# Kernel tuning notes

Hardware: AMD Instinct MI355X
Metric: run time of the kernel (lower is better)

Reference implementation:

```python
import jax, jax.numpy as jnp
import numpy as np

N, C, H, W = 4, 64, 64, 64
K = 3


def _unfold(x, k):
    """torch F.unfold with padding k//2: [n,c,h,w] -> [n, c*k*k, h*w].
    Feature ordering matches torch: index = c*k*k + i*k + j."""
    p = k // 2
    n, c, h, w = x.shape
    xp = jnp.pad(x, ((0, 0), (0, 0), (p, p), (p, p)))
    patches = jnp.stack(
        [xp[:, :, i:i + h, j:j + w] for i in range(k) for j in range(k)], axis=2
    )  # [n, c, k*k, h, w]
    return patches.reshape(n, c * k * k, h * w)


def _mask_vec(c, k):
    # causal patch mask from __init__: zero out center-and-right of middle row and all rows below
    m = np.ones((c, k, k), np.float32)
    m[:, k // 2, k // 2:] = 0
    m[:, k // 2 + 1:, :] = 0
    return jnp.asarray(m.reshape(1, c * k * k, 1))


def setup_inputs() -> dict:
    key = jax.random.key(0)
    k1, k2 = jax.random.split(key)
    y_hat = jax.random.normal(k1, (N, C, H, W), dtype=jnp.float32)
    y_prob = jax.random.uniform(k2, (N, 1, H, W), dtype=jnp.float32)
    return {"y_hat": y_hat, "y_prob": y_prob}


def reference(y_hat, y_prob):
    k = K
    n, c, h, w = y_hat.shape
    L = h * w
    mask = _mask_vec(c, k)

    u = _unfold(y_hat, k) * mask                              # [n, c*k*k, L]
    u = u / jnp.maximum(jnp.linalg.norm(u, axis=1, keepdims=True), 1e-12)
    R = jnp.einsum('nfl,nfm->nlm', u, u)                      # [n, L, L] cosine sims

    # eval path: keep strictly-upper triangle (causal: l < m)
    row = jnp.arange(L)[:, None]
    col = jnp.arange(L)[None, :]
    R = jnp.where(col > row, R, 0.0)

    R_star = jnp.max(R, axis=1)                               # [n, L]
    arg = jnp.argmax(R, axis=1).astype(jnp.int32)             # [n, L]

    y_unf = _unfold(y_hat, k)                                 # [n, c*k*k, L]
    ref_unfold = jnp.take_along_axis(y_unf, arg[:, None, :], axis=2)

    prob_unf = y_prob.reshape(n, -1, L)                       # 1x1 unfold
    U_unf = jnp.take_along_axis(prob_unf, arg[:, None, :], axis=2)

    S = R_star.reshape(n, 1, h, w)
    U = U_unf.reshape(n, -1, h, w)

    # eval-mode position-0 overrides
    S = S.at[:, :, 0, 0].set(1e-8)
    U = U.at[:, :, 0, 0].set(1e-8)
    ref_unfold = ref_unfold.at[:, :, 0].set(0.0)
    arg = arg.at[:, 0].set(-1)

    S = jnp.clip(S, 1e-8, 1.0)
    U = jnp.clip(U, 1e-8, 1.0)
    return S, U, ref_unfold, arg
```

## Files before the change

### kernel.cpp

```cpp
#include <hip/hip_runtime.h>
#include <stdint.h>

#define Nn 4
#define Cc 64
#define LL 4096
#define KK 256
#define TRI2 528

typedef _Float16 half8 __attribute__((ext_vector_type(8)));
typedef float f32x16 __attribute__((ext_vector_type(16)));
typedef float f4a __attribute__((ext_vector_type(4), aligned(4)));
typedef unsigned short ushort8v __attribute__((ext_vector_type(8)));

__device__ __forceinline__ unsigned f2ord(float f) {
    unsigned u = __float_as_uint(f);
    return u ^ ((u & 0x80000000u) ? 0xFFFFFFFFu : 0x80000000u);
}
__device__ __forceinline__ float ord2f(unsigned o) {
    unsigned u = (o & 0x80000000u) ? (o ^ 0x80000000u) : ~o;
    return __uint_as_float(u);
}
__device__ __forceinline__ unsigned short h2u(_Float16 h) {
    union { _Float16 f; unsigned short u; } x; x.f = h; return x.u;
}

__global__ __launch_bounds__(256) void build_v(const float* __restrict__ yhat,
                                               unsigned short* __restrict__ VhT,
                                               unsigned short* __restrict__ VlT,
                                               unsigned long long* __restrict__ best) {
    int blk = blockIdx.x;
    int xcd = blk & 7;
    int n = xcd >> 1;
    int i64 = (blk >> 3) + (xcd & 1) * 128;
    int tid = threadIdx.x;
    if (tid < 16) best[(size_t)n * LL + i64 * 16 + tid] = 0ull;

    int cg = tid & 15;
    int l = i64 * 16 + (tid >> 4);
    int y = l >> 6, x = l & 63;
    const float* src = yhat + (size_t)n * (Cc * LL);

    float vals[16];
    float sumsq = 0.f;
#pragma unroll
    for (int ci = 0; ci < 4; ++ci) {
        const float* p = src + (cg * 4 + ci) * LL;
        float t0 = (y > 0 && x > 0)  ? p[l - 65] : 0.f;
        float t1 = (y > 0)           ? p[l - 64] : 0.f;
        float t2 = (y > 0 && x < 63) ? p[l - 63] : 0.f;
        float t3 = (x > 0)           ? p[l - 1]  : 0.f;
        vals[ci * 4 + 0] = t0; vals[ci * 4 + 1] = t1;
        vals[ci * 4 + 2] = t2; vals[ci * 4 + 3] = t3;
        sumsq += t0 * t0 + t1 * t1 + t2 * t2 + t3 * t3;
    }
    sumsq += __shfl_xor(sumsq, 1, 64);
    sumsq += __shfl_xor(sumsq, 2, 64);
    sumsq += __shfl_xor(sumsq, 4, 64);
    sumsq += __shfl_xor(sumsq, 8, 64);
    float inv = 1.f / fmaxf(sqrtf(sumsq), 1e-12f);

    size_t pk = ((((size_t)n * 128 + (l >> 5)) * 16 + cg) << 9) + (l & 31) * 8;
    unsigned short* dh = VhT + pk;
    unsigned short* dl = VlT + pk;
    ushort8v hA, hB, lA, lB;
#pragma unroll
    for (int kk = 0; kk < 16; ++kk) {
        float v = vals[kk] * inv;
        _Float16 h = (fabsf(v) < 6.1035e-5f) ? (_Float16)0 : (_Float16)v;
        _Float16 lo = (_Float16)((v - (float)h) * 2048.0f);
        unsigned short hu = h2u(h * (_Float16)2048.0f);
        unsigned short lu = h2u(lo);
        if (kk < 8) { hA[kk] = hu; lA[kk] = lu; }
        else        { hB[kk - 8] = hu; lB[kk - 8] = lu; }
    }
    *(ushort8v*)(dh)       = hA;
    *(ushort8v*)(dh + 256) = hB;
    *(ushort8v*)(dl)       = lA;
    *(ushort8v*)(dl + 256) = lB;
}

__global__ __launch_bounds__(256) void simmax(const unsigned short* __restrict__ Vh,
                                              const unsigned short* __restrict__ Vl,
                                              unsigned long long* __restrict__ best) {
    int bx = blockIdx.x;
    int xcd = bx & 7, idx = bx >> 3;
    int n = xcd >> 1;
    int t = (xcd & 1) * 264 + idx;
    int j = (int)((sqrtf(8.f * (float)t + 1.f) - 1.f) * 0.5f);
    while ((j + 1) * (j + 2) / 2 <= t) ++j;
    while (j * (j + 1) / 2 > t) --j;
    int i = t - j * (j + 1) / 2;
    int l0 = i * 128, m0 = j * 128;

    int tid = threadIdx.x;
    int w = tid >> 6, lane = tid & 63;
    int r5 = lane & 31, h5 = lane >> 5;
    int rw = (w & 1) * 64;
    int cw = (w >> 1) * 64;
    if ((i == j) && (rw == 64) && (cw == 0)) return;

    const unsigned short* VhB = Vh + (size_t)n * (LL * KK);
    const unsigned short* VlB = Vl + (size_t)n * (LL * KK);

    const unsigned short* A_hi = VhB + ((size_t)((l0 + rw) >> 5) << 13) + lane * 8;
    const unsigned short* A_lo = VlB + ((size_t)((l0 + rw) >> 5) << 13) + lane * 8;
    const unsigned short* B_hi = VhB + ((size_t)((m0 + cw) >> 5) << 13) + lane * 8;
    const unsigned short* B_lo = VlB + ((size_t)((m0 + cw) >> 5) << 13) + lane * 8;

    f32x16 acc[2][2];
#pragma unroll
    for (int r = 0; r < 2; ++r)
#pragma unroll
        for (int c = 0; c < 2; ++c) acc[r][c] = (f32x16)0.f;

#pragma unroll 1
    for (int kb = 0; kb < 16; kb += 2) {
        half8 fal[2][2], fah[2][2], fbl[2][2], fbh[2][2];
#pragma unroll
        for (int kc = 0; kc < 2; ++kc)
#pragma unroll
            for (int r = 0; r < 2; ++r) {
                fal[r][kc] = *(const half8*)(A_lo + ((r * 16 + kb + kc) << 9));
                fbh[r][kc] = *(const half8*)(B_hi + ((r * 16 + kb + kc) << 9));
            }
#pragma unroll
        for (int kc = 0; kc < 2; ++kc)
#pragma unroll
            for (int r = 0; r < 2; ++r) {
                fah[r][kc] = *(const half8*)(A_hi + ((r * 16 + kb + kc) << 9));
                fbl[r][kc] = *(const half8*)(B_lo + ((r * 16 + kb + kc) << 9));
            }

        __builtin_amdgcn_s_setprio(1);
#pragma unroll
        for (int kc = 0; kc < 2; ++kc)
#pragma unroll
            for (int r = 0; r < 2; ++r)
#pragma unroll
                for (int c = 0; c < 2; ++c)
                    acc[r][c] = __builtin_amdgcn_mfma_f32_32x32x16_f16(fal[r][kc], fbh[c][kc], acc[r][c], 0, 0, 0);
#pragma unroll
        for (int kc = 0; kc < 2; ++kc)
#pragma unroll
            for (int r = 0; r < 2; ++r)
#pragma unroll
                for (int c = 0; c < 2; ++c)
                    acc[r][c] = __builtin_amdgcn_mfma_f32_32x32x16_f16(fah[r][kc], fbl[c][kc], acc[r][c], 0, 0, 0);
#pragma unroll
        for (int kc = 0; kc < 2; ++kc)
#pragma unroll
            for (int r = 0; r < 2; ++r)
#pragma unroll
                for (int c = 0; c < 2; ++c)
                    acc[r][c] = __builtin_amdgcn_mfma_f32_32x32x16_f16(fah[r][kc], fbh[c][kc], acc[r][c], 0, 0, 0);
        __builtin_amdgcn_s_setprio(0);
    }

    unsigned long long* bb = best + (size_t)n * LL;
    const float s = 1.f / 4194304.f;
#pragma unroll
    for (int c = 0; c < 2; ++c) {
        int m = m0 + cw + c * 32 + r5;
        unsigned long long key = 0ull;
#pragma unroll
        for (int r = 0; r < 2; ++r)
#pragma unroll
            for (int g = 0; g < 16; ++g) {
                int l = l0 + rw + r * 32 + (g & 3) + 8 * (g >> 2) + 4 * h5;
                if (l < m) {
                    float v = acc[r][c][g] * s;
                    unsigned long long k2 =
                        ((unsigned long long)f2ord(v) << 32) |
                        (unsigned long long)(0xFFFFFFFFu - (unsigned)l);
                    key = (k2 > key) ? k2 : key;
                }
            }
        unsigned long long o = __shfl_xor(key, 32, 64);
        key = (o > key) ? o : key;
        if (h5 == 0 && key != 0ull) atomicMax(bb + m, key);
    }
}

__global__ __launch_bounds__(256) void writeout(const float* __restrict__ yhat,
                                                const float* __restrict__ yprob,
                                                const unsigned long long* __restrict__ best,
                                                float* __restrict__ out) {
    int blk = blockIdx.x;
    int xcd = blk & 7;
    int n = xcd >> 1;
    int idx = (blk >> 3) + (xcd & 1) * 512;
    int mb = idx >> 4;
    int fc = idx & 15;
    int tid = threadIdx.x;
    int mm = tid & 63;
    int fs = tid >> 6;
    int c = fc * 4 + fs;
    int m = mb * 64 + mm;

    unsigned long long key = best[(size_t)n * LL + m];
    unsigned l = 0xFFFFFFFFu - (unsigned)(key & 0xFFFFFFFFull);
    float val = ord2f((unsigned)(key >> 32));
    bool zero = (m == 0);
    if (zero) l = 0;
    int ly = (int)(l >> 6), lx = (int)(l & 63);

    float* Sout = out;
    float* Uout = out + 16384;
    float* Rout = out + 32768;
    float* Aout = out + 9469952;

    if (fc == 0 && fs == 0) {
        float S = zero ? 1e-8f : fminf(fmaxf(val, 1e-8f), 1.0f);
        float U = zero ? 1e-8f : fminf(fmaxf(yprob[(size_t)n * LL + l], 1e-8f), 1.0f);
        Sout[(size_t)n * LL + m] = S;
        Uout[(size_t)n * LL + m] = U;
        Aout[(size_t)n * LL + m] = zero ? -1.0f : (float)l;
    }

    const float* src = yhat + (size_t)n * (Cc * LL);
    const float* plane = src + (size_t)c * LL;
    float* dst = Rout + (size_t)n * (576 * LL) + m;
    bool fast = (!zero) && (lx >= 1) && (lx <= 61);
#pragma unroll
    for (int r3 = 0; r3 < 3; ++r3) {
        int yy = ly + r3 - 1;
        bool rowok = (!zero) && (yy >= 0) && (yy < 64);
        float t0 = 0.f, t1 = 0.f, t2 = 0.f;
        if (rowok) {
            if (fast) {
                f4a v = *(const f4a*)(plane + yy * 64 + lx - 1);
                t0 = v.x; t1 = v.y; t2 = v.z;
            } else {
                if (lx > 0)  t0 = plane[yy * 64 + lx - 1];
                t1 = plane[yy * 64 + lx];
                if (lx < 63) t2 = plane[yy * 64 + lx + 1];
            }
        }
        size_t f = (size_t)(c * 9 + r3 * 3) * LL;
        __builtin_nontemporal_store(t0, dst + f);
        __builtin_nontemporal_store(t1, dst + f + LL);
        __builtin_nontemporal_store(t2, dst + f + 2 * (size_t)LL);
    }
}

extern "C" void kernel_launch(void* const* d_in, const int* in_sizes, int n_in,
                              void* d_out, int out_size, void* d_ws, size_t ws_size,
                              hipStream_t stream) {
    const float* yhat  = (const float*)d_in[0];
    const float* yprob = (const float*)d_in[1];
    float* out = (float*)d_out;

    unsigned short* VhT = (unsigned short*)d_ws;
    unsigned short* VlT = (unsigned short*)((char*)d_ws + 8388608);
    unsigned long long* best =
        (unsigned long long*)((char*)d_ws + 16777216);

    build_v<<<1024, 256, 0, stream>>>(yhat, VhT, VlT, best);
    simmax<<<Nn * TRI2, 256, 0, stream>>>(VhT, VlT, best);
    writeout<<<4096, 256, 0, stream>>>(yhat, yprob, best, out);
}
```

Before: 152.7 us.

## Transpose y_hat to channel-last, stage gather via LDS, double-buffer simmax loads

build_v now also writes a channel-last copy of y_hat, so writeout can gather each neighbor's 64 channels with vector loads. writeout stages a 16-position by 576-feature patch tile in shared memory and then writes 16 contiguous floats per feature row. The simmax main loop is restructured into explicit A/B register double-buffering with scalarized base pointers, so global loads overlap with the MFMAs. The costs are extra workspace traffic for the transposed copy, higher register pressure in simmax, and LDS use that may lower occupancy in writeout.

```diff
diff --git a/kernel.cpp b/kernel.cpp
--- a/kernel.cpp
+++ b/kernel.cpp
@@ -9,7 +9,7 @@
 
 typedef _Float16 half8 __attribute__((ext_vector_type(8)));
 typedef float f32x16 __attribute__((ext_vector_type(16)));
-typedef float f4a __attribute__((ext_vector_type(4), aligned(4)));
+typedef float f32x4 __attribute__((ext_vector_type(4)));
 typedef unsigned short ushort8v __attribute__((ext_vector_type(8)));
 
 __device__ __forceinline__ unsigned f2ord(float f) {
@@ -27,6 +27,7 @@
 __global__ __launch_bounds__(256) void build_v(const float* __restrict__ yhat,
                                                unsigned short* __restrict__ VhT,
                                                unsigned short* __restrict__ VlT,
+                                               float* __restrict__ yhatT,
                                                unsigned long long* __restrict__ best) {
     int blk = blockIdx.x;
     int xcd = blk & 7;
@@ -41,6 +42,7 @@
     const float* src = yhat + (size_t)n * (Cc * LL);
 
     float vals[16];
+    float ctr[4];
     float sumsq = 0.f;
 #pragma unroll
     for (int ci = 0; ci < 4; ++ci) {
@@ -49,6 +51,7 @@
         float t1 = (y > 0)           ? p[l - 64] : 0.f;
         float t2 = (y > 0 && x < 63) ? p[l - 63] : 0.f;
         float t3 = (x > 0)           ? p[l - 1]  : 0.f;
+        ctr[ci] = p[l];
         vals[ci * 4 + 0] = t0; vals[ci * 4 + 1] = t1;
         vals[ci * 4 + 2] = t2; vals[ci * 4 + 3] = t3;
         sumsq += t0 * t0 + t1 * t1 + t2 * t2 + t3 * t3;
@@ -58,6 +61,9 @@
     sumsq += __shfl_xor(sumsq, 4, 64);
     sumsq += __shfl_xor(sumsq, 8, 64);
     float inv = 1.f / fmaxf(sqrtf(sumsq), 1e-12f);
+
+    f32x4 cv; cv.x = ctr[0]; cv.y = ctr[1]; cv.z = ctr[2]; cv.w = ctr[3];
+    *(f32x4*)(yhatT + ((size_t)n * LL + l) * 64 + cg * 4) = cv;
 
     size_t pk = ((((size_t)n * 128 + (l >> 5)) * 16 + cg) << 9) + (l & 31) * 8;
     unsigned short* dh = VhT + pk;
@@ -77,6 +83,51 @@
     *(ushort8v*)(dh + 256) = hB;
     *(ushort8v*)(dl)       = lA;
     *(ushort8v*)(dl + 256) = lB;
+}
+
+__device__ __forceinline__ void loadset(const unsigned short* Ah0, const unsigned short* Ah1,
+                                        const unsigned short* Al0, const unsigned short* Al1,
+                                        const unsigned short* Bh0, const unsigned short* Bh1,
+                                        const unsigned short* Bl0, const unsigned short* Bl1,
+                                        int le,
+                                        half8 (&al)[2][2], half8 (&ah)[2][2],
+                                        half8 (&bl)[2][2], half8 (&bh)[2][2]) {
+    al[0][0] = *(const half8*)(Al0 + le);       al[0][1] = *(const half8*)(Al0 + 512 + le);
+    al[1][0] = *(const half8*)(Al1 + le);       al[1][1] = *(const half8*)(Al1 + 512 + le);
+    bh[0][0] = *(const half8*)(Bh0 + le);       bh[0][1] = *(const half8*)(Bh0 + 512 + le);
+    bh[1][0] = *(const half8*)(Bh1 + le);       bh[1][1] = *(const half8*)(Bh1 + 512 + le);
+    ah[0][0] = *(const half8*)(Ah0 + le);       ah[0][1] = *(const half8*)(Ah0 + 512 + le);
+    ah[1][0] = *(const half8*)(Ah1 + le);       ah[1][1] = *(const half8*)(Ah1 + 512 + le);
+    bl[0][0] = *(const half8*)(Bl0 + le);       bl[0][1] = *(const half8*)(Bl0 + 512 + le);
+    bl[1][0] = *(const half8*)(Bl1 + le);       bl[1][1] = *(const half8*)(Bl1 + 512 + le);
+}
+
+__device__ __forceinline__ void mfmaset(half8 (&al)[2][2], half8 (&ah)[2][2],
+                                        half8 (&bl)[2][2], half8 (&bh)[2][2],
+                                        f32x16 (&acc)[2][2]) {
+    __builtin_amdgcn_s_setprio(1);
+#pragma unroll
+    for (int kc = 0; kc < 2; ++kc)
+#pragma unroll
+        for (int r = 0; r < 2; ++r)
+#pragma unroll
+            for (int c = 0; c < 2; ++c)
+                acc[r][c] = __builtin_amdgcn_mfma_f32_32x32x16_f16(al[r][kc], bh[c][kc], acc[r][c], 0, 0, 0);
+#pragma unroll
+    for (int kc = 0; kc < 2; ++kc)
+#pragma unroll
+        for (int r = 0; r < 2; ++r)
+#pragma unroll
+            for (int c = 0; c < 2; ++c)
+                acc[r][c] = __builtin_amdgcn_mfma_f32_32x32x16_f16(ah[r][kc], bl[c][kc], acc[r][c], 0, 0, 0);
+#pragma unroll
+    for (int kc = 0; kc < 2; ++kc)
+#pragma unroll
+        for (int r = 0; r < 2; ++r)
+#pragma unroll
+            for (int c = 0; c < 2; ++c)
+                acc[r][c] = __builtin_amdgcn_mfma_f32_32x32x16_f16(ah[r][kc], bh[c][kc], acc[r][c], 0, 0, 0);
+    __builtin_amdgcn_s_setprio(0);
 }
 
 __global__ __launch_bounds__(256) void simmax(const unsigned short* __restrict__ Vh,
@@ -102,10 +153,17 @@
     const unsigned short* VhB = Vh + (size_t)n * (LL * KK);
     const unsigned short* VlB = Vl + (size_t)n * (LL * KK);
 
-    const unsigned short* A_hi = VhB + ((size_t)((l0 + rw) >> 5) << 13) + lane * 8;
-    const unsigned short* A_lo = VlB + ((size_t)((l0 + rw) >> 5) << 13) + lane * 8;
-    const unsigned short* B_hi = VhB + ((size_t)((m0 + cw) >> 5) << 13) + lane * 8;
-    const unsigned short* B_lo = VlB + ((size_t)((m0 + cw) >> 5) << 13) + lane * 8;
+    int aRow = __builtin_amdgcn_readfirstlane((l0 + rw) >> 5);
+    int bRow = __builtin_amdgcn_readfirstlane((m0 + cw) >> 5);
+    const unsigned short* Ah0 = VhB + ((size_t)aRow << 13);
+    const unsigned short* Ah1 = Ah0 + 8192;
+    const unsigned short* Al0 = VlB + ((size_t)aRow << 13);
+    const unsigned short* Al1 = Al0 + 8192;
+    const unsigned short* Bh0 = VhB + ((size_t)bRow << 13);
+    const unsigned short* Bh1 = Bh0 + 8192;
+    const unsigned short* Bl0 = VlB + ((size_t)bRow << 13);
+    const unsigned short* Bl1 = Bl0 + 8192;
+    int le = lane * 8;
 
     f32x16 acc[2][2];
 #pragma unroll
@@ -113,48 +171,26 @@
 #pragma unroll
         for (int c = 0; c < 2; ++c) acc[r][c] = (f32x16)0.f;
 
+    half8 alA[2][2], ahA[2][2], blA[2][2], bhA[2][2];
+    half8 alB[2][2], ahB[2][2], blB[2][2], bhB[2][2];
+
+#define BUMP() do { Ah0 += 1024; Ah1 += 1024; Al0 += 1024; Al1 += 1024; \
+                    Bh0 += 1024; Bh1 += 1024; Bl0 += 1024; Bl1 += 1024; } while (0)
+
+    loadset(Ah0, Ah1, Al0, Al1, Bh0, Bh1, Bl0, Bl1, le, alA, ahA, blA, bhA);
+    BUMP();
 #pragma unroll 1
-    for (int kb = 0; kb < 16; kb += 2) {
-        half8 fal[2][2], fah[2][2], fbl[2][2], fbh[2][2];
-#pragma unroll
-        for (int kc = 0; kc < 2; ++kc)
-#pragma unroll
-            for (int r = 0; r < 2; ++r) {
-                fal[r][kc] = *(const half8*)(A_lo + ((r * 16 + kb + kc) << 9));
-                fbh[r][kc] = *(const half8*)(B_hi + ((r * 16 + kb + kc) << 9));
-            }
-#pragma unroll
-        for (int kc = 0; kc < 2; ++kc)
-#pragma unroll
-            for (int r = 0; r < 2; ++r) {
-                fah[r][kc] = *(const half8*)(A_hi + ((r * 16 + kb + kc) << 9));
-                fbl[r][kc] = *(const half8*)(B_lo + ((r * 16 + kb + kc) << 9));
-            }
-
-        __builtin_amdgcn_s_setprio(1);
-#pragma unroll
-        for (int kc = 0; kc < 2; ++kc)
-#pragma unroll
-            for (int r = 0; r < 2; ++r)
-#pragma unroll
-                for (int c = 0; c < 2; ++c)
-                    acc[r][c] = __builtin_amdgcn_mfma_f32_32x32x16_f16(fal[r][kc], fbh[c][kc], acc[r][c], 0, 0, 0);
-#pragma unroll
-        for (int kc = 0; kc < 2; ++kc)
-#pragma unroll
-            for (int r = 0; r < 2; ++r)
-#pragma unroll
-                for (int c = 0; c < 2; ++c)
-                    acc[r][c] = __builtin_amdgcn_mfma_f32_32x32x16_f16(fah[r][kc], fbl[c][kc], acc[r][c], 0, 0, 0);
-#pragma unroll
-        for (int kc = 0; kc < 2; ++kc)
-#pragma unroll
-            for (int r = 0; r < 2; ++r)
-#pragma unroll
-                for (int c = 0; c < 2; ++c)
-                    acc[r][c] = __builtin_amdgcn_mfma_f32_32x32x16_f16(fah[r][kc], fbh[c][kc], acc[r][c], 0, 0, 0);
-        __builtin_amdgcn_s_setprio(0);
-    }
+    for (int it = 0; it < 4; ++it) {
+        loadset(Ah0, Ah1, Al0, Al1, Bh0, Bh1, Bl0, Bl1, le, alB, ahB, blB, bhB);
+        BUMP();
+        mfmaset(alA, ahA, blA, bhA, acc);
+        if (it < 3) {
+            loadset(Ah0, Ah1, Al0, Al1, Bh0, Bh1, Bl0, Bl1, le, alA, ahA, blA, bhA);
+            BUMP();
+        }
+        mfmaset(alB, ahB, blB, bhB, acc);
+    }
+#undef BUMP
 
     unsigned long long* bb = best + (size_t)n * LL;
     const float s = 1.f / 4194304.f;
@@ -181,21 +217,21 @@
     }
 }
 
-__global__ __launch_bounds__(256) void writeout(const float* __restrict__ yhat,
+__global__ __launch_bounds__(256) void writeout(const float* __restrict__ yhatT,
                                                 const float* __restrict__ yprob,
                                                 const unsigned long long* __restrict__ best,
                                                 float* __restrict__ out) {
+    __shared__ float P[576 * 17];
+
     int blk = blockIdx.x;
     int xcd = blk & 7;
     int n = xcd >> 1;
-    int idx = (blk >> 3) + (xcd & 1) * 512;
-    int mb = idx >> 4;
-    int fc = idx & 15;
+    int mb = (blk >> 3) + (xcd & 1) * 128;
+    int m0 = mb * 16;
     int tid = threadIdx.x;
-    int mm = tid & 63;
-    int fs = tid >> 6;
-    int c = fc * 4 + fs;
-    int m = mb * 64 + mm;
+    int ml = tid >> 4;
+    int cs = (tid & 15) * 4;
+    int m = m0 + ml;
 
     unsigned long long key = best[(size_t)n * LL + m];
     unsigned l = 0xFFFFFFFFu - (unsigned)(key & 0xFFFFFFFFull);
@@ -209,7 +245,7 @@
     float* Rout = out + 32768;
     float* Aout = out + 9469952;
 
-    if (fc == 0 && fs == 0) {
+    if (cs == 0) {
         float S = zero ? 1e-8f : fminf(fmaxf(val, 1e-8f), 1.0f);
         float U = zero ? 1e-8f : fminf(fmaxf(yprob[(size_t)n * LL + l], 1e-8f), 1.0f);
         Sout[(size_t)n * LL + m] = S;
@@ -217,29 +253,34 @@
         Aout[(size_t)n * LL + m] = zero ? -1.0f : (float)l;
     }
 
-    const float* src = yhat + (size_t)n * (Cc * LL);
-    const float* plane = src + (size_t)c * LL;
-    float* dst = Rout + (size_t)n * (576 * LL) + m;
-    bool fast = (!zero) && (lx >= 1) && (lx <= 61);
-#pragma unroll
-    for (int r3 = 0; r3 < 3; ++r3) {
-        int yy = ly + r3 - 1;
-        bool rowok = (!zero) && (yy >= 0) && (yy < 64);
-        float t0 = 0.f, t1 = 0.f, t2 = 0.f;
-        if (rowok) {
-            if (fast) {
-                f4a v = *(const f4a*)(plane + yy * 64 + lx - 1);
-                t0 = v.x; t1 = v.y; t2 = v.z;
-            } else {
-                if (lx > 0)  t0 = plane[yy * 64 + lx - 1];
-                t1 = plane[yy * 64 + lx];
-                if (lx < 63) t2 = plane[yy * 64 + lx + 1];
-            }
+    const float* T = yhatT + ((size_t)n * LL) * 64;
+#pragma unroll
+    for (int i = 0; i < 3; ++i) {
+        int yy = ly + i - 1;
+        bool rok = (!zero) && (yy >= 0) && (yy < 64);
+#pragma unroll
+        for (int jj = 0; jj < 3; ++jj) {
+            int xx = lx + jj - 1;
+            f32x4 v; v.x = 0.f; v.y = 0.f; v.z = 0.f; v.w = 0.f;
+            if (rok && xx >= 0 && xx < 64)
+                v = *(const f32x4*)(T + ((size_t)(yy * 64 + xx)) * 64 + cs);
+            int ij = i * 3 + jj;
+            P[((cs + 0) * 9 + ij) * 17 + ml] = v.x;
+            P[((cs + 1) * 9 + ij) * 17 + ml] = v.y;
+            P[((cs + 2) * 9 + ij) * 17 + ml] = v.z;
+            P[((cs + 3) * 9 + ij) * 17 + ml] = v.w;
         }
-        size_t f = (size_t)(c * 9 + r3 * 3) * LL;
-        __builtin_nontemporal_store(t0, dst + f);
-        __builtin_nontemporal_store(t1, dst + f + LL);
-        __builtin_nontemporal_store(t2, dst + f + 2 * (size_t)LL);
+    }
+    __syncthreads();
+
+    float* R = Rout + (size_t)n * (576 * LL) + m0;
+    int fl = tid >> 4;
+    int mm2 = tid & 15;
+#pragma unroll 1
+    for (int it2 = 0; it2 < 36; ++it2) {
+        int f = it2 * 16 + fl;
+        float v = P[f * 17 + mm2];
+        __builtin_nontemporal_store(v, R + (size_t)f * LL + mm2);
     }
 }
 
@@ -254,8 +295,9 @@
     unsigned short* VlT = (unsigned short*)((char*)d_ws + 8388608);
     unsigned long long* best =
         (unsigned long long*)((char*)d_ws + 16777216);
-
-    build_v<<<1024, 256, 0, stream>>>(yhat, VhT, VlT, best);
+    float* yhatT = (float*)((char*)d_ws + 16908288);
+
+    build_v<<<1024, 256, 0, stream>>>(yhat, VhT, VlT, yhatT, best);
     simmax<<<Nn * TRI2, 256, 0, stream>>>(VhT, VlT, best);
-    writeout<<<4096, 256, 0, stream>>>(yhat, yprob, best, out);
-}
+    writeout<<<1024, 256, 0, stream>>>(yhatT, yprob, best, out);
+}
```

Measured after the change: 156.4 us. +2.4%, slower.

## Stage shared A tile in LDS with double-buffered async loads, 8 waves per block

Applied to the files above, without the earlier changes.

The similarity-max kernel now runs 512 threads per 128x128 tile. Each wave owns a 64x32 sub-tile, and the A (row) operand is loaded once per block into double-buffered shared memory with global_load_lds. B fragments are prefetched into registers one k-step ahead. Tile ordering is changed to walk 4x4 super-blocks of the triangle, which should improve L2 reuse. The aim is to cut redundant global reads of A and overlap loads with MFMA work, at the cost of block-wide barriers each k-step and more complex wait-count logic that skipped waves must also take part in.

```diff
diff --git a/kernel.cpp b/kernel.cpp
--- a/kernel.cpp
+++ b/kernel.cpp
@@ -79,96 +79,161 @@
     *(ushort8v*)(dl + 256) = lB;
 }
 
-__global__ __launch_bounds__(256) void simmax(const unsigned short* __restrict__ Vh,
+__global__ __launch_bounds__(512) void simmax(const unsigned short* __restrict__ Vh,
                                               const unsigned short* __restrict__ Vl,
                                               unsigned long long* __restrict__ best) {
+    __shared__ __align__(16) unsigned short S[16384];
+
     int bx = blockIdx.x;
     int xcd = bx & 7, idx = bx >> 3;
     int n = xcd >> 1;
     int t = (xcd & 1) * 264 + idx;
-    int j = (int)((sqrtf(8.f * (float)t + 1.f) - 1.f) * 0.5f);
-    while ((j + 1) * (j + 2) / 2 <= t) ++j;
-    while (j * (j + 1) / 2 > t) --j;
-    int i = t - j * (j + 1) / 2;
+
+    int J = (int)((sqrtf(32.f * (float)t + 4.f) - 2.f) * 0.0625f);
+    while (8 * (J + 1) * (J + 1) + 2 * (J + 1) <= t) ++J;
+    while (8 * J * J + 2 * J > t) --J;
+    int r = t - (8 * J * J + 2 * J);
+    int i, j;
+    if (r < 16 * J) {
+        int I = r >> 4, inner = r & 15;
+        i = 4 * I + (inner & 3);
+        j = 4 * J + (inner >> 2);
+    } else {
+        int rr = r - 16 * J;
+        int dj = (rr >= 6) ? 3 : (rr >= 3) ? 2 : (rr >= 1) ? 1 : 0;
+        int di = rr - ((dj * (dj + 1)) >> 1);
+        i = 4 * J + di;
+        j = 4 * J + dj;
+    }
     int l0 = i * 128, m0 = j * 128;
 
     int tid = threadIdx.x;
-    int w = tid >> 6, lane = tid & 63;
+    int w = __builtin_amdgcn_readfirstlane(tid >> 6);
+    int lane = tid & 63;
     int r5 = lane & 31, h5 = lane >> 5;
     int rw = (w & 1) * 64;
-    int cw = (w >> 1) * 64;
-    if ((i == j) && (rw == 64) && (cw == 0)) return;
+    int cw = (w >> 1) * 32;
+    bool skip = (i == j) && (rw == 64) && (cw < 64);
 
     const unsigned short* VhB = Vh + (size_t)n * (LL * KK);
     const unsigned short* VlB = Vl + (size_t)n * (LL * KK);
 
-    const unsigned short* A_hi = VhB + ((size_t)((l0 + rw) >> 5) << 13) + lane * 8;
-    const unsigned short* A_lo = VlB + ((size_t)((l0 + rw) >> 5) << 13) + lane * 8;
-    const unsigned short* B_hi = VhB + ((size_t)((m0 + cw) >> 5) << 13) + lane * 8;
-    const unsigned short* B_lo = VlB + ((size_t)((m0 + cw) >> 5) << 13) + lane * 8;
-
-    f32x16 acc[2][2];
-#pragma unroll
-    for (int r = 0; r < 2; ++r)
-#pragma unroll
-        for (int c = 0; c < 2; ++c) acc[r][c] = (f32x16)0.f;
-
-#pragma unroll 1
-    for (int kb = 0; kb < 16; kb += 2) {
-        half8 fal[2][2], fah[2][2], fbl[2][2], fbh[2][2];
-#pragma unroll
-        for (int kc = 0; kc < 2; ++kc)
-#pragma unroll
-            for (int r = 0; r < 2; ++r) {
-                fal[r][kc] = *(const half8*)(A_lo + ((r * 16 + kb + kc) << 9));
-                fbh[r][kc] = *(const half8*)(B_hi + ((r * 16 + kb + kc) << 9));
+    int aRow0 = l0 >> 5;
+    int bRow0 = m0 >> 5;
+
+    int laneElem = lane * 8;
+
+    const unsigned short* gsrcA[2];
+    int lslotA[2];
+#pragma unroll
+    for (int q = 0; q < 2; ++q) {
+        int rb = w >> 1, lo = w & 1;
+        gsrcA[q] = (lo ? VlB : VhB) + ((size_t)((aRow0 + rb) * 16 + q) << 9) + laneElem;
+        lslotA[q] = (2 * w + q) * 512;
+    }
+    const unsigned short* pBh = VhB + ((size_t)((bRow0 + (w >> 1)) * 16) << 9) + laneElem;
+    const unsigned short* pBl = VlB + ((size_t)((bRow0 + (w >> 1)) * 16) << 9) + laneElem;
+
+    int arb = (w & 1) * 2;
+
+    f32x16 acc[2];
+#pragma unroll
+    for (int r2 = 0; r2 < 2; ++r2) acc[r2] = (f32x16)0.f;
+
+#define GLDSA(KQ, BN)                                                             \
+    do {                                                                          \
+        _Pragma("unroll")                                                         \
+        for (int q = 0; q < 2; ++q)                                               \
+            __builtin_amdgcn_global_load_lds(                                     \
+                (const __attribute__((address_space(1))) void*)(gsrcA[q] + (size_t)(KQ) * 1024), \
+                (__attribute__((address_space(3))) void*)(S + (BN) * 8192 + lslotA[q]), 16, 0, 0); \
+    } while (0)
+
+#define MFMA_SET(AL, AH, BH, BL)                                                  \
+    do {                                                                          \
+        __builtin_amdgcn_s_setprio(1);                                            \
+        _Pragma("unroll")                                                         \
+        for (int kc = 0; kc < 2; ++kc)                                            \
+            _Pragma("unroll")                                                     \
+            for (int r2 = 0; r2 < 2; ++r2)                                        \
+                acc[r2] = __builtin_amdgcn_mfma_f32_32x32x16_f16((AL)[r2][kc], (BH)[kc], acc[r2], 0, 0, 0); \
+        _Pragma("unroll")                                                         \
+        for (int kc = 0; kc < 2; ++kc)                                            \
+            _Pragma("unroll")                                                     \
+            for (int r2 = 0; r2 < 2; ++r2)                                        \
+                acc[r2] = __builtin_amdgcn_mfma_f32_32x32x16_f16((AH)[r2][kc], (BL)[kc], acc[r2], 0, 0, 0); \
+        _Pragma("unroll")                                                         \
+        for (int kc = 0; kc < 2; ++kc)                                            \
+            _Pragma("unroll")                                                     \
+            for (int r2 = 0; r2 < 2; ++r2)                                        \
+                acc[r2] = __builtin_amdgcn_mfma_f32_32x32x16_f16((AH)[r2][kc], (BH)[kc], acc[r2], 0, 0, 0); \
+        __builtin_amdgcn_s_setprio(0);                                            \
+    } while (0)
+
+    half8 bhP[2], blP[2], bhQ[2], blQ[2];
+
+    GLDSA(0, 0);
+    __builtin_amdgcn_sched_barrier(0);
+    if (!skip) {
+        bhP[0] = *(const half8*)(pBh);        bhP[1] = *(const half8*)(pBh + 512);
+        blP[0] = *(const half8*)(pBl);        blP[1] = *(const half8*)(pBl + 512);
+    }
+
+#pragma unroll
+    for (int kq = 0; kq < 8; ++kq) {
+        const int cur = (kq & 1) * 8192;
+        const bool even = (kq & 1) == 0;
+
+        if (skip) { asm volatile("s_waitcnt lgkmcnt(0) vmcnt(0)" ::: "memory"); }
+        else      { asm volatile("s_waitcnt lgkmcnt(0) vmcnt(4)" ::: "memory"); }
+        __builtin_amdgcn_s_barrier();
+        __builtin_amdgcn_sched_barrier(0);
+
+        if (kq < 7) {
+            GLDSA(kq + 1, (kq + 1) & 1);
+            __builtin_amdgcn_sched_barrier(0);
+            if (!skip) {
+                const unsigned short* nh = pBh + (size_t)(kq + 1) * 1024;
+                const unsigned short* nl = pBl + (size_t)(kq + 1) * 1024;
+                if (even) {
+                    bhQ[0] = *(const half8*)(nh);       bhQ[1] = *(const half8*)(nh + 512);
+                    blQ[0] = *(const half8*)(nl);       blQ[1] = *(const half8*)(nl + 512);
+                } else {
+                    bhP[0] = *(const half8*)(nh);       bhP[1] = *(const half8*)(nh + 512);
+                    blP[0] = *(const half8*)(nl);       blP[1] = *(const half8*)(nl + 512);
+                }
             }
-#pragma unroll
-        for (int kc = 0; kc < 2; ++kc)
-#pragma unroll
-            for (int r = 0; r < 2; ++r) {
-                fah[r][kc] = *(const half8*)(A_hi + ((r * 16 + kb + kc) << 9));
-                fbl[r][kc] = *(const half8*)(B_lo + ((r * 16 + kb + kc) << 9));
-            }
-
-        __builtin_amdgcn_s_setprio(1);
-#pragma unroll
-        for (int kc = 0; kc < 2; ++kc)
-#pragma unroll
-            for (int r = 0; r < 2; ++r)
-#pragma unroll
-                for (int c = 0; c < 2; ++c)
-                    acc[r][c] = __builtin_amdgcn_mfma_f32_32x32x16_f16(fal[r][kc], fbh[c][kc], acc[r][c], 0, 0, 0);
-#pragma unroll
-        for (int kc = 0; kc < 2; ++kc)
-#pragma unroll
-            for (int r = 0; r < 2; ++r)
-#pragma unroll
-                for (int c = 0; c < 2; ++c)
-                    acc[r][c] = __builtin_amdgcn_mfma_f32_32x32x16_f16(fah[r][kc], fbl[c][kc], acc[r][c], 0, 0, 0);
-#pragma unroll
-        for (int kc = 0; kc < 2; ++kc)
-#pragma unroll
-            for (int r = 0; r < 2; ++r)
-#pragma unroll
-                for (int c = 0; c < 2; ++c)
-                    acc[r][c] = __builtin_amdgcn_mfma_f32_32x32x16_f16(fah[r][kc], fbh[c][kc], acc[r][c], 0, 0, 0);
-        __builtin_amdgcn_s_setprio(0);
-    }
-
+        }
+
+        if (!skip) {
+            half8 al[2][2], ah[2][2];
+#pragma unroll
+            for (int kc = 0; kc < 2; ++kc)
+#pragma unroll
+                for (int r2 = 0; r2 < 2; ++r2) {
+                    al[r2][kc] = *(const half8*)(S + cur + (((arb + r2) * 2 + 1) * 2 + kc) * 512 + laneElem);
+                    ah[r2][kc] = *(const half8*)(S + cur + (((arb + r2) * 2) * 2 + kc) * 512 + laneElem);
+                }
+            if (even) MFMA_SET(al, ah, bhP, blP);
+            else      MFMA_SET(al, ah, bhQ, blQ);
+        }
+    }
+#undef GLDSA
+#undef MFMA_SET
+
+    if (skip) return;
     unsigned long long* bb = best + (size_t)n * LL;
     const float s = 1.f / 4194304.f;
-#pragma unroll
-    for (int c = 0; c < 2; ++c) {
-        int m = m0 + cw + c * 32 + r5;
+    {
+        int m = m0 + cw + r5;
         unsigned long long key = 0ull;
 #pragma unroll
-        for (int r = 0; r < 2; ++r)
+        for (int r2 = 0; r2 < 2; ++r2)
 #pragma unroll
             for (int g = 0; g < 16; ++g) {
-                int l = l0 + rw + r * 32 + (g & 3) + 8 * (g >> 2) + 4 * h5;
+                int l = l0 + rw + r2 * 32 + (g & 3) + 8 * (g >> 2) + 4 * h5;
                 if (l < m) {
-                    float v = acc[r][c][g] * s;
+                    float v = acc[r2][g] * s;
                     unsigned long long k2 =
                         ((unsigned long long)f2ord(v) << 32) |
                         (unsigned long long)(0xFFFFFFFFu - (unsigned)l);
@@ -256,6 +321,6 @@
         (unsigned long long*)((char*)d_ws + 16777216);
 
     build_v<<<1024, 256, 0, stream>>>(yhat, VhT, VlT, best);
-    simmax<<<Nn * TRI2, 256, 0, stream>>>(VhT, VlT, best);
+    simmax<<<Nn * TRI2, 512, 0, stream>>>(VhT, VlT, best);
     writeout<<<4096, 256, 0, stream>>>(yhat, yprob, best, out);
 }
```

After: 150.4 us. Within noise of the previous version (-1.5%).
